# Kernel tuning notes

Measured on AMD Instinct MI355X. Metric: run time of the kernel, lower is better.

Reference implementation:

```python
import jax, jax.numpy as jnp
import numpy as np

B, S, DM = 1, 2048, 2048
H, KV, DH = 32, 8, 64
ROT, DQ = 32, 16  # rotary dims; DQ = ROT // 2
GROUPS = H // KV


def setup_inputs() -> dict:
    key = jax.random.key(0)
    ks = jax.random.split(key, 9)
    sc = 0.02
    hidden_states = jax.random.normal(ks[0], (B, S, DM), jnp.float32)
    # realistic RoPE tables: theta = pos * inv_freq, shape [1,1,S,DQ] (broadcasts over heads)
    inv_freq = 1.0 / (10000.0 ** (jnp.arange(DQ, dtype=jnp.float32) / DQ))
    ang = jnp.arange(S, dtype=jnp.float32)[:, None] * inv_freq[None, :]
    cos = jnp.cos(ang)[None, None]
    sin = jnp.sin(ang)[None, None]
    position_ids = jnp.broadcast_to(jnp.arange(S, dtype=jnp.int64 if jax.config.read('jax_enable_x64') else jnp.int32), (B, S))
    Wq = jax.random.normal(ks[1], (DM, H * DH), jnp.float32) * sc
    Wk = jax.random.normal(ks[2], (DM, KV * DH), jnp.float32) * sc
    Wv = jax.random.normal(ks[3], (DM, KV * DH), jnp.float32) * sc
    Wo = jax.random.normal(ks[4], (H * DH, DM), jnp.float32) * sc
    qkv_dim = H * DH + 2 * KV * DH
    tau_Wq = jax.random.normal(ks[5], (qkv_dim, H), jnp.float32) * sc
    tau_Wv = jax.random.normal(ks[6], (qkv_dim, H), jnp.float32) * sc
    tau_alpha = jax.random.normal(ks[7], (H,), jnp.float32)
    return {"hidden_states": hidden_states, "cos": cos, "sin": sin,
            "position_ids": position_ids, "Wq": Wq, "Wk": Wk, "Wv": Wv,
            "Wo": Wo, "tau_Wq": tau_Wq, "tau_Wv": tau_Wv, "tau_alpha": tau_alpha}


def _rope(x, cos, sin):
    # x: [B, h, S, DH]; rotate first ROT dims (half-split real/imag), interleave output
    x_rot, x_pass = x[..., :ROT], x[..., ROT:]
    xr, xi = x_rot[..., :DQ], x_rot[..., DQ:]
    out_r = xr * cos - xi * sin
    out_i = xr * sin + xi * cos
    out = jnp.stack([out_r, out_i], axis=-1).reshape(x.shape[:-1] + (ROT,))
    return jnp.concatenate([out, x_pass], axis=-1)


def reference(hidden_states, cos, sin, position_ids, Wq, Wk, Wv, Wo, tau_Wq, tau_Wv, tau_alpha):
    b, s, _ = hidden_states.shape
    q = hidden_states @ Wq                      # [B,S,H*DH]
    k = hidden_states @ Wk                      # [B,S,KV*DH]
    v = hidden_states @ Wv                      # [B,S,KV*DH]
    # tau gating: gelu(concat qkv) -> tanh projections -> position sigmoid term
    feat = jax.nn.gelu(jnp.concatenate([q, k, v], axis=-1), approximate=False)
    tok_q = jnp.tanh(feat @ tau_Wq).transpose(0, 2, 1)   # [B,H,S]
    tok_v = jnp.tanh(feat @ tau_Wv).transpose(0, 2, 1)   # [B,H,S]
    pos = position_ids.astype(hidden_states.dtype) + 1.0
    tau_pos = 1.0 + (jax.nn.sigmoid(tau_alpha[None, :, None] * jnp.log(pos)[:, None, :]) - 0.5)
    tau_q = (tok_q + tau_pos)[..., None]        # [B,H,S,1]
    tau_v = (tok_v + tau_pos)[..., None]        # [B,H,S,1]
    q = q.reshape(b, s, H, DH).transpose(0, 2, 1, 3) * tau_q   # [B,H,S,DH]
    k = k.reshape(b, s, KV, DH).transpose(0, 2, 1, 3)          # [B,KV,S,DH]
    # torch: tau_v.repeat(1,groups,1,1)[:, :KV] == first KV heads of tau_v
    v = v.reshape(b, s, KV, DH).transpose(0, 2, 1, 3) * tau_v[:, :KV]
    q = _rope(q, cos, sin)
    k = _rope(k, cos, sin)
    # GQA expand kv heads, causal SDPA
    k = jnp.repeat(k, GROUPS, axis=1)
    v = jnp.repeat(v, GROUPS, axis=1)
    scores = jnp.einsum('bhqd,bhkd->bhqk', q, k) / np.sqrt(DH).astype(np.float32)
    causal = jnp.tril(jnp.ones((s, s), dtype=bool))
    scores = jnp.where(causal, scores, jnp.finfo(scores.dtype).min)
    attn = jax.nn.softmax(scores, axis=-1)
    out = jnp.einsum('bhqk,bhkd->bhqd', attn, v)
    out = out.transpose(0, 2, 1, 3).reshape(b, s, H * DH)
    return out @ Wo
```

## Files before the change

kernel.cpp:

```cpp
#include <hip/hip_runtime.h>
#include <cmath>

typedef __bf16 bf16x8 __attribute__((ext_vector_type(8)));
typedef __bf16 bf16x4 __attribute__((ext_vector_type(4)));
typedef float f32x4 __attribute__((ext_vector_type(4)));
typedef unsigned short u16;
typedef unsigned int u32;

__device__ __forceinline__ u16 f2bf(float f) {
  union { float f; unsigned int u; } v; v.f = f;
  unsigned int u = v.u;
  return (u16)((u + 0x7FFFu + ((u >> 16) & 1u)) >> 16);
}

__device__ __forceinline__ float geluf(float x) {
  return 0.5f * x * (1.0f + erff(x * 0.7071067811865475f));
}

__device__ __forceinline__ void gl_lds16(const void* g, void* l) {
  __builtin_amdgcn_global_load_lds(
      (const __attribute__((address_space(1))) u32*)g,
      (__attribute__((address_space(3))) u32*)l, 16, 0, 0);
}

__global__ __launch_bounds__(256) void cvt_bf16(const float* __restrict__ in,
                                                u16* __restrict__ out, int n8) {
  int i = blockIdx.x * 256 + threadIdx.x;
  if (i >= n8) return;
  const float4* p = (const float4*)in + 2 * (size_t)i;
  float4 a = p[0], b = p[1];
  uint4 o;
  o.x = (unsigned)f2bf(a.x) | ((unsigned)f2bf(a.y) << 16);
  o.y = (unsigned)f2bf(a.z) | ((unsigned)f2bf(a.w) << 16);
  o.z = (unsigned)f2bf(b.x) | ((unsigned)f2bf(b.y) << 16);
  o.w = (unsigned)f2bf(b.z) | ((unsigned)f2bf(b.w) << 16);
  ((uint4*)out)[i] = o;
}

__global__ __launch_bounds__(256) void transpose_all(const float* __restrict__ Wq,
                                                     const float* __restrict__ Wk,
                                                     const float* __restrict__ Wv,
                                                     const float* __restrict__ Wo,
                                                     const float* __restrict__ tWq,
                                                     const float* __restrict__ tWv,
                                                     u16* __restrict__ WqkvT,
                                                     u16* __restrict__ WoT,
                                                     u16* __restrict__ Tt) {
  __shared__ float tile[64][65];
  int b = blockIdx.x;
  const float* in; u16* out; int R, C, bx, by;
  if (b < 1024)      { in = Wq;  out = WqkvT;                R = 2048; C = 2048; bx = b & 31; by = b >> 5; }
  else if (b < 1280) { b -= 1024; in = Wk; out = WqkvT + 2048ull * 2048; R = 2048; C = 512; bx = b & 7; by = b >> 3; }
  else if (b < 1536) { b -= 1280; in = Wv; out = WqkvT + 2560ull * 2048; R = 2048; C = 512; bx = b & 7; by = b >> 3; }
  else if (b < 2560) { b -= 1536; in = Wo; out = WoT;        R = 2048; C = 2048; bx = b & 31; by = b >> 5; }
  else if (b < 2608) { b -= 2560; in = tWq; out = Tt;               R = 3072; C = 32; bx = 0; by = b; }
  else               { b -= 2608; in = tWv; out = Tt + 32ull * 3072; R = 3072; C = 32; bx = 0; by = b; }

  const int t = threadIdx.x;
  const int r0 = by * 64, c0 = bx * 64;
  const int lr = t >> 4, lc4 = (t & 15) * 4;
#pragma unroll
  for (int p = 0; p < 4; ++p) {
    int r = p * 16 + lr;
    float4 v = {0.f, 0.f, 0.f, 0.f};
    if (c0 + lc4 < C) v = *(const float4*)(in + (size_t)(r0 + r) * C + c0 + lc4);
    tile[r][lc4] = v.x; tile[r][lc4 + 1] = v.y;
    tile[r][lc4 + 2] = v.z; tile[r][lc4 + 3] = v.w;
  }
  __syncthreads();
  const int cg = t >> 4, rr4 = (t & 15) * 4;
#pragma unroll
  for (int p = 0; p < 4; ++p) {
    int c = p * 16 + cg;
    if (c0 + c < C) {
      uint2 w;
      w.x = (u32)f2bf(tile[rr4][c])     | ((u32)f2bf(tile[rr4 + 1][c]) << 16);
      w.y = (u32)f2bf(tile[rr4 + 2][c]) | ((u32)f2bf(tile[rr4 + 3][c]) << 16);
      *(uint2*)(out + (size_t)(c0 + c) * R + r0 + rr4) = w;
    }
  }
}

template <int WR, int WC>
__global__ __launch_bounds__(256, 3) void gemm_bt(const u16* __restrict__ A,
                                                  const u16* __restrict__ Bt,
                                                  float* __restrict__ Cpart,
                                                  int M, int N, int K, int kPer) {
  constexpr int BM = WR * 64, BN = WC * 64;
  __shared__ __attribute__((aligned(16))) u16 As[BM * 64];
  __shared__ __attribute__((aligned(16))) u16 Bs[BN * 64];
  const int tid = threadIdx.x, wid = tid >> 6, lane = tid & 63;
  const int l16 = lane & 15, quad = lane >> 4;
  const int wm = (wid % WR) * 64, wn = (wid / WR) * 64;
  const int m0 = blockIdx.y * BM, n0 = blockIdx.x * BN;
  const int kIters = K >> 6;
  const int kStart = blockIdx.z * kPer;
  const int kEnd = (kStart + kPer < kIters) ? (kStart + kPer) : kIters;

  const int lrow = lane >> 3;
  const int swz = (lane & 7) ^ lrow;
  const u16* gAb = A + (size_t)m0 * K + (size_t)swz * 8;
  const u16* gBb = Bt + (size_t)n0 * K + (size_t)swz * 8;
  const int sx = l16 & 7;

  f32x4 acc[4][4] = {};
  for (int kt = kStart; kt < kEnd; ++kt) {
    __syncthreads();
    const u16* gA = gAb + (size_t)kt * 64;
    const u16* gB = gBb + (size_t)kt * 64;
#pragma unroll
    for (int j = 0; j < BM / 32; ++j) {
      int i = wid * (BM / 32) + j;
      gl_lds16(gA + (size_t)(i * 8 + lrow) * K, &As[i * 512]);
    }
#pragma unroll
    for (int j = 0; j < BN / 32; ++j) {
      int i = wid * (BN / 32) + j;
      gl_lds16(gB + (size_t)(i * 8 + lrow) * K, &Bs[i * 512]);
    }
    __syncthreads();
    bf16x8 af[4][2], bfr[4][2];
#pragma unroll
    for (int mt = 0; mt < 4; ++mt)
#pragma unroll
      for (int ks = 0; ks < 2; ++ks)
        af[mt][ks] = *(const bf16x8*)(&As[(wm + mt * 16 + l16) * 64 +
                                          (((ks * 4 + quad) ^ sx) * 8)]);
#pragma unroll
    for (int nt = 0; nt < 4; ++nt)
#pragma unroll
      for (int ks = 0; ks < 2; ++ks)
        bfr[nt][ks] = *(const bf16x8*)(&Bs[(wn + nt * 16 + l16) * 64 +
                                           (((ks * 4 + quad) ^ sx) * 8)]);
#pragma unroll
    for (int mt = 0; mt < 4; ++mt)
#pragma unroll
      for (int nt = 0; nt < 4; ++nt)
#pragma unroll
        for (int ks = 0; ks < 2; ++ks)
          acc[mt][nt] = __builtin_amdgcn_mfma_f32_16x16x32_bf16(
              af[mt][ks], bfr[nt][ks], acc[mt][nt], 0, 0, 0);
  }

  float* C = Cpart + (size_t)blockIdx.z * M * N;
#pragma unroll
  for (int mt = 0; mt < 4; ++mt)
#pragma unroll
    for (int nt = 0; nt < 4; ++nt)
#pragma unroll
      for (int r = 0; r < 4; ++r) {
        int row = m0 + wm + mt * 16 + quad * 4 + r;
        int col = n0 + wn + nt * 16 + l16;
        C[(size_t)row * N + col] = acc[mt][nt][r];
      }
}

__global__ __launch_bounds__(256) void reduce_gelu(float* __restrict__ base, int P,
                                                   int n4, u16* __restrict__ gout) {
  int i = blockIdx.x * 256 + threadIdx.x;
  if (i >= n4) return;
  size_t n = (size_t)n4 * 4;
  float4 v = ((const float4*)base)[i];
  for (int p = 1; p < P; ++p) {
    float4 w = ((const float4*)(base + (size_t)p * n))[i];
    v.x += w.x; v.y += w.y; v.z += w.z; v.w += w.w;
  }
  if (P > 1) ((float4*)base)[i] = v;
  uint2 o;
  o.x = (u32)f2bf(geluf(v.x)) | ((u32)f2bf(geluf(v.y)) << 16);
  o.y = (u32)f2bf(geluf(v.z)) | ((u32)f2bf(geluf(v.w)) << 16);
  ((uint2*)gout)[i] = o;
}

__global__ __launch_bounds__(256) void reduce_add(const float* __restrict__ base, int P,
                                                  int n4, float* __restrict__ dst) {
  int i = blockIdx.x * 256 + threadIdx.x;
  if (i >= n4) return;
  size_t n = (size_t)n4 * 4;
  float4 v = ((const float4*)base)[i];
  for (int p = 1; p < P; ++p) {
    float4 w = ((const float4*)(base + (size_t)p * n))[i];
    v.x += w.x; v.y += w.y; v.z += w.z; v.w += w.w;
  }
  ((float4*)dst)[i] = v;
}

__global__ __launch_bounds__(256) void reduce_tanh(const float* __restrict__ base, int P,
                                                   int n, float* __restrict__ tokq,
                                                   float* __restrict__ tokv) {
  int i = blockIdx.x * 256 + threadIdx.x;
  if (i >= n) return;
  float v = base[i];
  for (int p = 1; p < P; ++p) v += base[(size_t)p * n + i];
  float t = tanhf(v);
  int col = i & 63, row = i >> 6;
  if (col < 32) tokq[row * 32 + col] = t;
  else          tokv[row * 32 + (col - 32)] = t;
}

#define QSCALE 0.18033688011112042f
__global__ __launch_bounds__(256) void prep_qkv(const float* __restrict__ qkv,
                                                const float* __restrict__ tokq,
                                                const float* __restrict__ tokv,
                                                const float* __restrict__ alpha,
                                                const float* __restrict__ cosb,
                                                const float* __restrict__ sinb,
                                                const int* __restrict__ pos_ids,
                                                u16* __restrict__ Qb,
                                                u16* __restrict__ Kb,
                                                u16* __restrict__ Vt,
                                                u16* __restrict__ Vb) {
  const int s = blockIdx.x;
  const int tid = threadIdx.x;
  __shared__ float cs[16], sn[16], tq_s[32], tv_s[32];
  if (tid < 16) { cs[tid] = cosb[s * 16 + tid]; sn[tid] = sinb[s * 16 + tid]; }
  if (tid < 32) {
    float p = (float)pos_ids[s] + 1.0f;
    float sig = 1.0f / (1.0f + __expf(-alpha[tid] * logf(p)));
    float taupos = 0.5f + sig;
    tq_s[tid] = (tokq[s * 32 + tid] + taupos) * QSCALE;
    tv_s[tid] = tokv[s * 32 + tid] + taupos;
  }
  __syncthreads();
  const float* row = qkv + (size_t)s * 3072;

  for (int idx = tid; idx < 2048; idx += 256) {
    int h = idx >> 6, d = idx & 63;
    float tq = tq_s[h];
    float v;
    if (d < 32) {
      int i = d >> 1;
      float xr = row[h * 64 + i] * tq, xi = row[h * 64 + 16 + i] * tq;
      v = (d & 1) ? (xr * sn[i] + xi * cs[i]) : (xr * cs[i] - xi * sn[i]);
    } else v = row[h * 64 + d] * tq;
    Qb[((size_t)h * 2048 + s) * 64 + d] = f2bf(v);
  }
  for (int idx = tid; idx < 512; idx += 256) {
    int h = idx >> 6, d = idx & 63;
    const float* kr = row + 2048;
    float v;
    if (d < 32) {
      int i = d >> 1;
      float xr = kr[h * 64 + i], xi = kr[h * 64 + 16 + i];
      v = (d & 1) ? (xr * sn[i] + xi * cs[i]) : (xr * cs[i] - xi * sn[i]);
    } else v = kr[h * 64 + d];
    Kb[((size_t)h * 2048 + s) * 64 + d] = f2bf(v);
  }
  for (int idx = tid; idx < 512; idx += 256) {
    int h = idx >> 6, d = idx & 63;
    float v = row[2560 + h * 64 + d] * tv_s[h];
    u16 b = f2bf(v);
    if (Vb) Vb[((size_t)h * 2048 + s) * 64 + d] = b;
    else    Vt[((size_t)h * 64 + d) * 2048 + s] = b;
  }
}

__global__ __launch_bounds__(256) void vtrans(const u16* __restrict__ Vb,
                                              u16* __restrict__ Vt) {
  __shared__ u16 t[64][68];
  const int s0 = blockIdx.x * 64, h = blockIdx.y;
  const int tid = threadIdx.x;
  const u16* src = Vb + ((size_t)h * 2048 + s0) * 64;
#pragma unroll
  for (int p = 0; p < 4; ++p) {
    int v = p * 256 + tid;
    int r = v >> 4, c = (v & 15) * 4;
    uint2 w = *(const uint2*)(src + (size_t)r * 64 + c);
    t[r][c] = (u16)(w.x & 0xffff); t[r][c + 1] = (u16)(w.x >> 16);
    t[r][c + 2] = (u16)(w.y & 0xffff); t[r][c + 3] = (u16)(w.y >> 16);
  }
  __syncthreads();
  u16* dst = Vt + (size_t)h * 64 * 2048 + s0;
#pragma unroll
  for (int p = 0; p < 4; ++p) {
    int v = p * 256 + tid;
    int d = v >> 4, s = (v & 15) * 4;
    uint2 w;
    w.x = (u32)t[s][d] | ((u32)t[s + 1][d] << 16);
    w.y = (u32)t[s + 2][d] | ((u32)t[s + 3][d] << 16);
    *(uint2*)(dst + (size_t)d * 2048 + s) = w;
  }
}

__global__ __launch_bounds__(256, 3) void flash_attn(const u16* __restrict__ Qb,
                                                     const u16* __restrict__ Kb,
                                                     const u16* __restrict__ Vt,
                                                     float* __restrict__ Opart,
                                                     float* __restrict__ ml) {
  __shared__ __attribute__((aligned(16))) u16 KsB[2][4096];
  __shared__ __attribute__((aligned(16))) u16 VsB[2][4096];
  __shared__ __attribute__((aligned(16))) u16 Ps[128 * 64];
  const int e = 50 - blockIdx.x;
  const int h = blockIdx.y, kvh = h >> 2;
  int a = 0;
  while (3 * (a + 1) * (a + 2) / 2 <= e) ++a;
  const int rem = e - 3 * a * (a + 1) / 2;
  const int qb = 3 * a + rem / (a + 1);
  const int cc = rem % (a + 1);
  const int k0 = cc * 6;
  const int kvTend = 2 * qb + 2;
  const int k1 = (k0 + 6 < kvTend) ? (k0 + 6) : kvTend;
  const int pid = h * 51 + e;

  const int tid = threadIdx.x, wid = tid >> 6, lane = tid & 63;
  const int l16 = lane & 15, quad = lane >> 4;
  const int lrow = lane >> 3, swz = (lane & 7) ^ lrow, sx = l16 & 7;

  const int q0 = qb * 128 + wid * 32;
  bf16x8 qf[2][2];
#pragma unroll
  for (int mt = 0; mt < 2; ++mt)
#pragma unroll
    for (int ks = 0; ks < 2; ++ks)
      qf[mt][ks] = *(const bf16x8*)(Qb + ((size_t)h * 2048 + q0 + mt * 16 + l16) * 64 +
                                    ks * 32 + quad * 8);

  f32x4 oacc[2][4] = {};
  float mrun[2] = {-3e38f, -3e38f};
  float lrun[2] = {0.f, 0.f};

  const u16* kgb = Kb + ((size_t)kvh * 2048) * 64;
  const u16* vgb = Vt + (size_t)kvh * 64 * 2048;

#define FA_STAGE(KT, BUF)                                                         \
  {                                                                               \
    const u16* kg_ = kgb + (size_t)(KT)*64 * 64;                                  \
    const u16* vg_ = vgb + (size_t)(KT)*64;                                       \
    _Pragma("unroll") for (int j = 0; j < 2; ++j) {                               \
      int i_ = wid * 2 + j;                                                       \
      gl_lds16(kg_ + (size_t)(i_ * 8 + lrow) * 64 + swz * 8, &KsB[BUF][i_ * 512]);\
      gl_lds16(vg_ + (size_t)(i_ * 8 + lrow) * 2048 + swz * 8, &VsB[BUF][i_ * 512]);\
    }                                                                             \
  }

  FA_STAGE(k0, 0)
  for (int kt = k0; kt < k1; ++kt) {
    const int cur = (kt - k0) & 1;
    __syncthreads();
    if (kt + 1 < k1) FA_STAGE(kt + 1, cur ^ 1)
    const u16* Ks = KsB[cur];
    const u16* Vs = VsB[cur];

    f32x4 sacc[2][4] = {};
#pragma unroll
    for (int kf = 0; kf < 4; ++kf) {
      bf16x8 a0 = *(const bf16x8*)(Ks + (kf * 16 + l16) * 64 + ((quad ^ sx) << 3));
      bf16x8 a1 = *(const bf16x8*)(Ks + (kf * 16 + l16) * 64 + (((4 + quad) ^ sx) << 3));
      sacc[0][kf] = __builtin_amdgcn_mfma_f32_16x16x32_bf16(a0, qf[0][0], sacc[0][kf], 0, 0, 0);
      sacc[0][kf] = __builtin_amdgcn_mfma_f32_16x16x32_bf16(a1, qf[0][1], sacc[0][kf], 0, 0, 0);
      sacc[1][kf] = __builtin_amdgcn_mfma_f32_16x16x32_bf16(a0, qf[1][0], sacc[1][kf], 0, 0, 0);
      sacc[1][kf] = __builtin_amdgcn_mfma_f32_16x16x32_bf16(a1, qf[1][1], sacc[1][kf], 0, 0, 0);
    }

    const bool msk = (kt >= 2 * qb);
#pragma unroll
    for (int mt = 0; mt < 2; ++mt) {
      const int qg = q0 + mt * 16 + l16;
      if (msk) {
        const int kb = kt * 64 + quad * 4;
#pragma unroll
        for (int kf = 0; kf < 4; ++kf)
#pragma unroll
          for (int r = 0; r < 4; ++r)
            if (kb + kf * 16 + r > qg) sacc[mt][kf][r] = -1e9f;
      }
      f32x4 m4 = sacc[mt][0];
      m4 = __builtin_elementwise_max(m4, sacc[mt][1]);
      m4 = __builtin_elementwise_max(m4, sacc[mt][2]);
      m4 = __builtin_elementwise_max(m4, sacc[mt][3]);
      float mx = fmaxf(fmaxf(m4[0], m4[1]), fmaxf(m4[2], m4[3]));
      mx = fmaxf(mx, __shfl_xor(mx, 16));
      mx = fmaxf(mx, __shfl_xor(mx, 32));
      float mn = fmaxf(mrun[mt], mx);
      float al = __builtin_amdgcn_exp2f(mrun[mt] - mn);
      mrun[mt] = mn;
      float ps = 0.f;
      const int prow = wid * 32 + mt * 16 + l16;
      u16* prp = Ps + prow * 64 + ((quad & 1) << 2);
      const int pswz = prow & 7;
#pragma unroll
      for (int kf = 0; kf < 4; ++kf) {
        bf16x4 pk;
#pragma unroll
        for (int r = 0; r < 4; ++r) {
          float p = __builtin_amdgcn_exp2f(sacc[mt][kf][r] - mn);
          ps += p;
          pk[r] = (__bf16)p;
        }
        *(bf16x4*)(prp + (((kf * 2 + (quad >> 1)) ^ pswz) << 3)) = pk;
      }
      ps += __shfl_xor(ps, 16);
      ps += __shfl_xor(ps, 32);
      lrun[mt] = lrun[mt] * al + ps;
#pragma unroll
      for (int df = 0; df < 4; ++df) oacc[mt][df] *= al;
    }

#pragma unroll
    for (int ks = 0; ks < 2; ++ks) {
      const int q0r = wid * 32 + l16, q1r = q0r + 16;
      bf16x8 b0 = *(const bf16x8*)(Ps + q0r * 64 + (((ks * 4 + quad) ^ (q0r & 7)) << 3));
      bf16x8 b1 = *(const bf16x8*)(Ps + q1r * 64 + (((ks * 4 + quad) ^ (q1r & 7)) << 3));
#pragma unroll
      for (int df = 0; df < 4; ++df) {
        bf16x8 va = *(const bf16x8*)(Vs + (df * 16 + l16) * 64 + (((ks * 4 + quad) ^ sx) << 3));
        oacc[0][df] = __builtin_amdgcn_mfma_f32_16x16x32_bf16(va, b0, oacc[0][df], 0, 0, 0);
        oacc[1][df] = __builtin_amdgcn_mfma_f32_16x16x32_bf16(va, b1, oacc[1][df], 0, 0, 0);
      }
    }
  }
#undef FA_STAGE

  float* Op = Opart + (size_t)pid * 128 * 64;
#pragma unroll
  for (int mt = 0; mt < 2; ++mt) {
    const int qrow = wid * 32 + mt * 16 + l16;
#pragma unroll
    for (int df = 0; df < 4; ++df)
      *(f32x4*)(Op + (size_t)qrow * 64 + df * 16 + quad * 4) = oacc[mt][df];
    if (quad == 0) {
      ml[((size_t)pid * 128 + qrow) * 2] = mrun[mt];
      ml[((size_t)pid * 128 + qrow) * 2 + 1] = lrun[mt];
    }
  }
}

__global__ __launch_bounds__(256) void fa_combine(const float* __restrict__ Opart,
                                                  const float* __restrict__ ml,
                                                  u16* __restrict__ Ob) {
  const int qb = blockIdx.x, h = blockIdx.y;
  const int C = (2 * qb + 7) / 6;
  const int aa = qb / 3, bb = qb % 3;
  const int base = h * 51 + 3 * aa * (aa + 1) / 2 + bb * (aa + 1);
  const int t = threadIdx.x;
#pragma unroll
  for (int u = 0; u < 8; ++u) {
    int unit = u * 256 + t;
    int row = unit >> 4, d4 = unit & 15;
    float mstar = -3e38f;
    for (int c = 0; c < C; ++c)
      mstar = fmaxf(mstar, ml[((size_t)(base + c) * 128 + row) * 2]);
    float4 o = {0.f, 0.f, 0.f, 0.f};
    float lsum = 0.f;
    for (int c = 0; c < C; ++c) {
      const float* mlp = &ml[((size_t)(base + c) * 128 + row) * 2];
      float w = __builtin_amdgcn_exp2f(mlp[0] - mstar);
      float4 v = ((const float4*)(Opart + ((size_t)(base + c) * 128 + row) * 64))[d4];
      o.x += w * v.x; o.y += w * v.y; o.z += w * v.z; o.w += w * v.w;
      lsum += w * mlp[1];
    }
    float inv = 1.0f / lsum;
    uint2 pk;
    pk.x = (u32)f2bf(o.x * inv) | ((u32)f2bf(o.y * inv) << 16);
    pk.y = (u32)f2bf(o.z * inv) | ((u32)f2bf(o.w * inv) << 16);
    *(uint2*)(Ob + (size_t)(qb * 128 + row) * 2048 + h * 64 + d4 * 4) = pk;
  }
}

extern "C" void kernel_launch(void* const* d_in, const int* in_sizes, int n_in,
                              void* d_out, int out_size, void* d_ws, size_t ws_size,
                              hipStream_t stream) {
  (void)in_sizes; (void)n_in; (void)out_size;
  const float* hidden = (const float*)d_in[0];
  const float* cosb   = (const float*)d_in[1];
  const float* sinb   = (const float*)d_in[2];
  const int*   pos    = (const int*)d_in[3];
  const float* Wq     = (const float*)d_in[4];
  const float* Wk     = (const float*)d_in[5];
  const float* Wv     = (const float*)d_in[6];
  const float* Wo     = (const float*)d_in[7];
  const float* tWq    = (const float*)d_in[8];
  const float* tWv    = (const float*)d_in[9];
  const float* alpha  = (const float*)d_in[10];
  float* out = (float*)d_out;

  const bool big = ws_size >= (size_t)120 * 1024 * 1024;
  const int Pq = big ? 2 : 1;
  const int Pt = big ? 16 : 1;
  const int Po = big ? 3 : 1;

  char* ws = (char*)d_ws;
  size_t off = 0;
  auto alloc = [&](size_t bytes) -> void* {
    void* p = ws + off;
    off += (bytes + 255) & ~(size_t)255;
    return p;
  };
  u16*   WoT   = (u16*)alloc(2048ull * 2048 * 2);
  u16*   Tt    = (u16*)alloc(64ull * 3072 * 2);
  u16*   Qb    = (u16*)alloc(32ull * 2048 * 64 * 2);
  u16*   Kb    = (u16*)alloc(8ull * 2048 * 64 * 2);
  u16*   Vt    = (u16*)alloc(8ull * 64 * 2048 * 2);
  u16*   Ob    = (u16*)alloc(2048ull * 2048 * 2);
  u16*   featb = (u16*)alloc(2048ull * 3072 * 2);
  float* tokq  = (float*)alloc(2048ull * 32 * 4);
  float* tokv  = (float*)alloc(2048ull * 32 * 4);
  u16*   Vb    = big ? (u16*)alloc(8ull * 2048 * 64 * 2) : nullptr;
  size_t E = off;
  u16*   Xb      = (u16*)alloc(2048ull * 2048 * 2);
  u16*   WqkvT   = (u16*)alloc(3072ull * 2048 * 2);
  float* qkvPart = (float*)alloc((size_t)Pq * 2048 * 3072 * 4);
  float* qkv     = qkvPart;
  float* tokPart = (float*)(ws + E);
  float* Opart   = (float*)(ws + E);
  float* mlbuf   = (float*)(ws + E + 1632ull * 128 * 64 * 4);
  float* outPart = (float*)(ws + E);

  cvt_bf16<<<2048, 256, 0, stream>>>(hidden, Xb, 2048 * 2048 / 8);
  transpose_all<<<2656, 256, 0, stream>>>(Wq, Wk, Wv, Wo, tWq, tWv, WqkvT, WoT, Tt);

  gemm_bt<2, 2><<<dim3(24, 16, Pq), 256, 0, stream>>>(
      Xb, WqkvT, qkvPart, 2048, 3072, 2048, (32 + Pq - 1) / Pq);
  reduce_gelu<<<6144, 256, 0, stream>>>(qkvPart, Pq, 2048 * 3072 / 4, featb);

  gemm_bt<4, 1><<<dim3(1, 8, Pt), 256, 0, stream>>>(
      featb, Tt, tokPart, 2048, 64, 3072, (48 + Pt - 1) / Pt);
  reduce_tanh<<<512, 256, 0, stream>>>(tokPart, Pt, 2048 * 64, tokq, tokv);

  prep_qkv<<<2048, 256, 0, stream>>>(qkv, tokq, tokv, alpha, cosb, sinb, pos,
                                     Qb, Kb, Vt, Vb);
  if (big) vtrans<<<dim3(32, 8), 256, 0, stream>>>(Vb, Vt);

  flash_attn<<<dim3(51, 32), 256, 0, stream>>>(Qb, Kb, Vt, Opart, mlbuf);
  fa_combine<<<dim3(16, 32), 256, 0, stream>>>(Opart, mlbuf, Ob);

  gemm_bt<2, 2><<<dim3(16, 16, Po), 256, 0, stream>>>(
      Ob, WoT, outPart, 2048, 2048, 2048, (32 + Po - 1) / Po);
  reduce_add<<<4096, 256, 0, stream>>>(outPart, Po, 2048 * 2048 / 4, out);
}
```

Baseline: 286.7 us.

## Keep softmax probabilities in registers and feed PV with 16x16x16 MFMA

The flash-attention kernel no longer writes P to a shared-memory tile and reads it back. The S accumulator layout is reused directly as the B operand of 16x16x16 bf16 MFMAs, with V fragments read at matching offsets. The row-sum shuffle reductions move out of the loop to the epilogue, s_setprio is raised around the MFMA blocks, and the occupancy hint goes from 3 to 4 blocks per CU. This removes LDS traffic and a round-trip through shared memory, but uses twice as many smaller MFMA instructions for PV and may add register pressure at the higher occupancy target.

```diff
diff --git a/kernel.cpp b/kernel.cpp
--- a/kernel.cpp
+++ b/kernel.cpp
@@ -4,6 +4,7 @@
 typedef __bf16 bf16x8 __attribute__((ext_vector_type(8)));
 typedef __bf16 bf16x4 __attribute__((ext_vector_type(4)));
 typedef float f32x4 __attribute__((ext_vector_type(4)));
+typedef short s16x4 __attribute__((ext_vector_type(4)));
 typedef unsigned short u16;
 typedef unsigned int u32;
 
@@ -15,6 +16,17 @@
 
 __device__ __forceinline__ float geluf(float x) {
   return 0.5f * x * (1.0f + erff(x * 0.7071067811865475f));
+}
+
+__device__ __forceinline__ f32x4 mfma_16x16x16_bf16(s16x4 a, s16x4 b, f32x4 c) {
+#if __has_builtin(__builtin_amdgcn_mfma_f32_16x16x16bf16_1k)
+  return __builtin_amdgcn_mfma_f32_16x16x16bf16_1k(a, b, c, 0, 0, 0);
+#else
+  f32x4 d;
+  asm volatile("v_mfma_f32_16x16x16_bf16 %0, %1, %2, %3"
+               : "=v"(d) : "v"(a), "v"(b), "0"(c));
+  return d;
+#endif
 }
 
 __device__ __forceinline__ void gl_lds16(const void* g, void* l) {
@@ -282,14 +294,13 @@
   }
 }
 
-__global__ __launch_bounds__(256, 3) void flash_attn(const u16* __restrict__ Qb,
+__global__ __launch_bounds__(256, 4) void flash_attn(const u16* __restrict__ Qb,
                                                      const u16* __restrict__ Kb,
                                                      const u16* __restrict__ Vt,
                                                      float* __restrict__ Opart,
                                                      float* __restrict__ ml) {
   __shared__ __attribute__((aligned(16))) u16 KsB[2][4096];
   __shared__ __attribute__((aligned(16))) u16 VsB[2][4096];
-  __shared__ __attribute__((aligned(16))) u16 Ps[128 * 64];
   const int e = 50 - blockIdx.x;
   const int h = blockIdx.y, kvh = h >> 2;
   int a = 0;
@@ -342,6 +353,7 @@
     const u16* Vs = VsB[cur];
 
     f32x4 sacc[2][4] = {};
+    __builtin_amdgcn_s_setprio(1);
 #pragma unroll
     for (int kf = 0; kf < 4; ++kf) {
       bf16x8 a0 = *(const bf16x8*)(Ks + (kf * 16 + l16) * 64 + ((quad ^ sx) << 3));
@@ -351,8 +363,10 @@
       sacc[1][kf] = __builtin_amdgcn_mfma_f32_16x16x32_bf16(a0, qf[1][0], sacc[1][kf], 0, 0, 0);
       sacc[1][kf] = __builtin_amdgcn_mfma_f32_16x16x32_bf16(a1, qf[1][1], sacc[1][kf], 0, 0, 0);
     }
+    __builtin_amdgcn_s_setprio(0);
 
     const bool msk = (kt >= 2 * qb);
+    s16x4 pb[2][4];
 #pragma unroll
     for (int mt = 0; mt < 2; ++mt) {
       const int qg = q0 + mt * 16 + l16;
@@ -374,53 +388,53 @@
       float mn = fmaxf(mrun[mt], mx);
       float al = __builtin_amdgcn_exp2f(mrun[mt] - mn);
       mrun[mt] = mn;
-      float ps = 0.f;
-      const int prow = wid * 32 + mt * 16 + l16;
-      u16* prp = Ps + prow * 64 + ((quad & 1) << 2);
-      const int pswz = prow & 7;
+      float psl = 0.f;
 #pragma unroll
       for (int kf = 0; kf < 4; ++kf) {
-        bf16x4 pk;
+        bf16x4 ph;
 #pragma unroll
         for (int r = 0; r < 4; ++r) {
           float p = __builtin_amdgcn_exp2f(sacc[mt][kf][r] - mn);
-          ps += p;
-          pk[r] = (__bf16)p;
+          psl += p;
+          ph[r] = (__bf16)p;
         }
-        *(bf16x4*)(prp + (((kf * 2 + (quad >> 1)) ^ pswz) << 3)) = pk;
+        union { bf16x4 h; s16x4 s; } cv;
+        cv.h = ph;
+        pb[mt][kf] = cv.s;
       }
-      ps += __shfl_xor(ps, 16);
-      ps += __shfl_xor(ps, 32);
-      lrun[mt] = lrun[mt] * al + ps;
+      lrun[mt] = lrun[mt] * al + psl;
 #pragma unroll
       for (int df = 0; df < 4; ++df) oacc[mt][df] *= al;
     }
 
-#pragma unroll
-    for (int ks = 0; ks < 2; ++ks) {
-      const int q0r = wid * 32 + l16, q1r = q0r + 16;
-      bf16x8 b0 = *(const bf16x8*)(Ps + q0r * 64 + (((ks * 4 + quad) ^ (q0r & 7)) << 3));
-      bf16x8 b1 = *(const bf16x8*)(Ps + q1r * 64 + (((ks * 4 + quad) ^ (q1r & 7)) << 3));
+    __builtin_amdgcn_s_setprio(1);
+#pragma unroll
+    for (int kf = 0; kf < 4; ++kf) {
 #pragma unroll
       for (int df = 0; df < 4; ++df) {
-        bf16x8 va = *(const bf16x8*)(Vs + (df * 16 + l16) * 64 + (((ks * 4 + quad) ^ sx) << 3));
-        oacc[0][df] = __builtin_amdgcn_mfma_f32_16x16x32_bf16(va, b0, oacc[0][df], 0, 0, 0);
-        oacc[1][df] = __builtin_amdgcn_mfma_f32_16x16x32_bf16(va, b1, oacc[1][df], 0, 0, 0);
+        s16x4 va = *(const s16x4*)(Vs + (df * 16 + l16) * 64 +
+                                   (((kf * 2 + (quad >> 1)) ^ sx) << 3) + ((quad & 1) << 2));
+        oacc[0][df] = mfma_16x16x16_bf16(va, pb[0][kf], oacc[0][df]);
+        oacc[1][df] = mfma_16x16x16_bf16(va, pb[1][kf], oacc[1][df]);
       }
     }
+    __builtin_amdgcn_s_setprio(0);
   }
 #undef FA_STAGE
 
   float* Op = Opart + (size_t)pid * 128 * 64;
 #pragma unroll
   for (int mt = 0; mt < 2; ++mt) {
+    float lt = lrun[mt];
+    lt += __shfl_xor(lt, 16);
+    lt += __shfl_xor(lt, 32);
     const int qrow = wid * 32 + mt * 16 + l16;
 #pragma unroll
     for (int df = 0; df < 4; ++df)
       *(f32x4*)(Op + (size_t)qrow * 64 + df * 16 + quad * 4) = oacc[mt][df];
     if (quad == 0) {
       ml[((size_t)pid * 128 + qrow) * 2] = mrun[mt];
-      ml[((size_t)pid * 128 + qrow) * 2 + 1] = lrun[mt];
+      ml[((size_t)pid * 128 + qrow) * 2 + 1] = lt;
     }
   }
 }
```

Result: slower. 292.7 us (+2.1%).
